# Performance work log

Measured on AMD Instinct MI355X. Metric: run time of the kernel, lower is better.

## Reference

```python
import jax, jax.numpy as jnp
import numpy as np

B, L, DIM, H = 1, 2048, 1536, 12
HD = DIM // H  # 128
SCALE = HD ** -0.5


def quantize_dequant_int8(t):
    # per-tensor symmetric int8 quantize then float dequantize (same math as torch ref)
    s = jnp.max(jnp.abs(t)) / 127.0
    q = jnp.clip(jnp.round(t / s), -128.0, 127.0)
    return q * s


def setup_inputs() -> dict:
    key = jax.random.key(0)
    ks = jax.random.split(key, 6)
    std = DIM ** -0.5
    return {
        "x": jax.random.normal(ks[0], (B, L, DIM), jnp.float32),
        "Wq": jax.random.normal(ks[1], (DIM, DIM), jnp.float32) * std,
        "Wk": jax.random.normal(ks[2], (DIM, DIM), jnp.float32) * std,
        "Wv": jax.random.normal(ks[3], (DIM, DIM), jnp.float32) * std,
        "Wo": jax.random.normal(ks[4], (DIM, DIM), jnp.float32) * std,
        "bo": jax.random.normal(ks[5], (DIM,), jnp.float32) * 0.01,
    }


def reference(x, Wq, Wk, Wv, Wo, bo):
    b, l, c = x.shape
    # QKV projections (torch Linear: x @ W^T), reshape to [B,H,L,HD]
    q = (x @ Wq.T).reshape(b, l, H, HD).transpose(0, 2, 1, 3)
    k = (x @ Wk.T).reshape(b, l, H, HD).transpose(0, 2, 1, 3)
    v = (x @ Wv.T).reshape(b, l, H, HD).transpose(0, 2, 1, 3)
    # sage-style quantize/dequant around both matmuls
    qd = quantize_dequant_int8(q)
    kd = quantize_dequant_int8(k)
    scores = jnp.einsum('bhqd,bhkd->bhqk', qd, kd) * SCALE
    probs = jax.nn.softmax(scores, axis=-1)
    pd = quantize_dequant_int8(probs)
    vd = quantize_dequant_int8(v)
    out = jnp.einsum('bhqk,bhkd->bhqd', pd, vd)  # [B,H,L,HD]
    out = out.transpose(0, 2, 1, 3).reshape(b, l, c)
    return out @ Wo.T + bo
```

## Files before the change

### kernel.cpp

```cpp
#include <hip/hip_runtime.h>
#include <stdint.h>

#define SEQ 2048
#define DIM 1536
#define NH  12
#define HD  128
#define SCALEF 0.08838834764831845f
#define LDP 40

typedef __attribute__((ext_vector_type(8))) short short8;
typedef __attribute__((ext_vector_type(4))) float floatx4;

#define MFMA16(a, b, c) __builtin_amdgcn_mfma_f32_16x16x32_bf16((a), (b), (c), 0, 0, 0)

__device__ __forceinline__ void async_cp16(const void* g, void* l) {
  __builtin_amdgcn_global_load_lds(
      (__attribute__((address_space(1))) unsigned int*)(g),
      (__attribute__((address_space(3))) unsigned int*)(l), 16, 0, 0);
}

__device__ __forceinline__ unsigned short f2bf(float f) {
  unsigned int u = __float_as_uint(f);
  u = (u + 0x7fff + ((u >> 16) & 1)) >> 16;
  return (unsigned short)u;
}

__device__ __forceinline__ void split8v(const float* x, short8& h, short8& l) {
#pragma unroll
  for (int e = 0; e < 8; e++) {
    unsigned int u = __float_as_uint(x[e]);
    h[e] = (short)(u >> 16);
    float r = x[e] - __uint_as_float(u & 0xFFFF0000u);
    l[e] = (short)f2bf(r);
  }
}
__device__ __forceinline__ void split8(const float* g, short8& h, short8& l) {
  float4 f0 = *(const float4*)g, f1 = *(const float4*)(g + 4);
  float x[8] = {f0.x, f0.y, f0.z, f0.w, f1.x, f1.y, f1.z, f1.w};
  split8v(x, h, l);
}

__global__ __launch_bounds__(256) void k_fill(float* __restrict__ out, int n,
                                              float val) {
  int i = blockIdx.x * 256 + threadIdx.x;
  if (i < n) out[i] = val;
}

__global__ __launch_bounds__(256) void k_split_x(
    const float* __restrict__ X, unsigned short* __restrict__ Xh,
    unsigned short* __restrict__ Xl) {
  size_t i = ((size_t)blockIdx.x * 256 + threadIdx.x) * 8;
  short8 h, l;
  split8(X + i, h, l);
  *(short8*)(Xh + i) = h;
  *(short8*)(Xl + i) = l;
}

__global__ __launch_bounds__(256) void k_split_o(
    const float* __restrict__ A0, const float* __restrict__ A1,
    unsigned short* __restrict__ Oh, unsigned short* __restrict__ Ol) {
  size_t i = ((size_t)blockIdx.x * 256 + threadIdx.x) * 8;
  float4 x0 = *(const float4*)(A0 + i), x1 = *(const float4*)(A0 + i + 4);
  float4 y0 = *(const float4*)(A1 + i), y1 = *(const float4*)(A1 + i + 4);
  float xs[8] = {x0.x + y0.x, x0.y + y0.y, x0.z + y0.z, x0.w + y0.w,
                 x1.x + y1.x, x1.y + y1.y, x1.z + y1.z, x1.w + y1.w};
  short8 h, l;
  split8v(xs, h, l);
  *(short8*)(Oh + i) = h;
  *(short8*)(Ol + i) = l;
}

__global__ __launch_bounds__(256) void k_gemm_qkv(
    const unsigned short* __restrict__ Xh, const unsigned short* __restrict__ Xl,
    const float* __restrict__ Wq, const float* __restrict__ Wk,
    const float* __restrict__ Wv, float* __restrict__ qf,
    float* __restrict__ kf, float* __restrict__ vf,
    unsigned int* __restrict__ scal) {
  __shared__ __align__(16) unsigned short Ahs[2][128 * 32], Als[2][128 * 32];
  __shared__ __align__(16) unsigned short Bh[2][128 * LDP], Bl[2][128 * LDP];
  int tid = threadIdx.x, z = blockIdx.z;
  const float* W = (z == 0) ? Wq : (z == 1) ? Wk : Wv;
  float* C = (z == 0) ? qf : (z == 1) ? kf : vf;
  int n0 = blockIdx.x * 128, m0 = blockIdx.y * 128;
  int lane = tid & 63, w = tid >> 6;
  int wr = w >> 1, wc = w & 1, lm = lane & 15, q = lane >> 4;

  floatx4 acc[4][4];
#pragma unroll
  for (int i = 0; i < 4; i++)
#pragma unroll
    for (int j = 0; j < 4; j++) acc[i][j] = (floatx4){0.f, 0.f, 0.f, 0.f};

  int rowA = tid >> 2, c8 = tid & 3;
  const float* pB0 = W + (size_t)(n0 + rowA) * DIM + c8 * 8;
  const float* pB1 = pB0 + (size_t)64 * DIM;
  int sidx0 = tid, sidx1 = 256 + tid;
  int smr0 = sidx0 >> 2, sq0 = (sidx0 & 3) ^ ((smr0 >> 1) & 3);
  int smr1 = sidx1 >> 2, sq1 = (sidx1 & 3) ^ ((smr1 >> 1) & 3);
  size_t gofA0 = (size_t)(m0 + smr0) * DIM + sq0 * 8;
  size_t gofA1 = (size_t)(m0 + smr1) * DIM + sq1 * 8;
  int phA = (q ^ ((lm >> 1) & 3)) * 8;
  int mrbase = wr * 64 + lm;

  {
    async_cp16(Xh + gofA0, &Ahs[0][0] + sidx0 * 8);
    async_cp16(Xl + gofA0, &Als[0][0] + sidx0 * 8);
    async_cp16(Xh + gofA1, &Ahs[0][0] + sidx1 * 8);
    async_cp16(Xl + gofA1, &Als[0][0] + sidx1 * 8);
    short8 h, l;
    split8(pB0, h, l);
    *(short8*)(&Bh[0][0] + rowA * LDP + c8 * 8) = h;
    *(short8*)(&Bl[0][0] + rowA * LDP + c8 * 8) = l;
    split8(pB1, h, l);
    *(short8*)(&Bh[0][0] + (64 + rowA) * LDP + c8 * 8) = h;
    *(short8*)(&Bl[0][0] + (64 + rowA) * LDP + c8 * 8) = l;
  }
  __syncthreads();

  for (int it = 0; it < 47; ++it) {
    int cur = it & 1, nxt = cur ^ 1;
    int kn = it * 32 + 32;
    float4 b00 = *(const float4*)(pB0 + kn);
    float4 b01 = *(const float4*)(pB0 + kn + 4);
    float4 b10 = *(const float4*)(pB1 + kn);
    float4 b11 = *(const float4*)(pB1 + kn + 4);
    async_cp16(Xh + gofA0 + kn, &Ahs[nxt][0] + sidx0 * 8);
    async_cp16(Xl + gofA0 + kn, &Als[nxt][0] + sidx0 * 8);
    async_cp16(Xh + gofA1 + kn, &Ahs[nxt][0] + sidx1 * 8);
    async_cp16(Xl + gofA1 + kn, &Als[nxt][0] + sidx1 * 8);
    short8 ah[4], al[4], bh[4], bl[4];
#pragma unroll
    for (int i = 0; i < 4; i++) {
      int off = (mrbase + i * 16) * 32 + phA;
      ah[i] = *(const short8*)(&Ahs[cur][0] + off);
      al[i] = *(const short8*)(&Als[cur][0] + off);
    }
#pragma unroll
    for (int j = 0; j < 4; j++) {
      int r = wc * 64 + j * 16 + lm;
      bh[j] = *(const short8*)(&Bh[cur][0] + r * LDP + q * 8);
      bl[j] = *(const short8*)(&Bl[cur][0] + r * LDP + q * 8);
    }
#pragma unroll
    for (int i = 0; i < 4; i++)
#pragma unroll
      for (int j = 0; j < 4; j++) {
        acc[i][j] = MFMA16(ah[i], bh[j], acc[i][j]);
        acc[i][j] = MFMA16(ah[i], bl[j], acc[i][j]);
        acc[i][j] = MFMA16(al[i], bh[j], acc[i][j]);
      }
    {
      short8 h, l;
      {
        float xs[8] = {b00.x, b00.y, b00.z, b00.w, b01.x, b01.y, b01.z, b01.w};
        split8v(xs, h, l);
        *(short8*)(&Bh[nxt][0] + rowA * LDP + c8 * 8) = h;
        *(short8*)(&Bl[nxt][0] + rowA * LDP + c8 * 8) = l;
      }
      {
        float xs[8] = {b10.x, b10.y, b10.z, b10.w, b11.x, b11.y, b11.z, b11.w};
        split8v(xs, h, l);
        *(short8*)(&Bh[nxt][0] + (64 + rowA) * LDP + c8 * 8) = h;
        *(short8*)(&Bl[nxt][0] + (64 + rowA) * LDP + c8 * 8) = l;
      }
    }
    __syncthreads();
  }
  {
    short8 ah[4], al[4], bh[4], bl[4];
#pragma unroll
    for (int i = 0; i < 4; i++) {
      int off = (mrbase + i * 16) * 32 + phA;
      ah[i] = *(const short8*)(&Ahs[1][0] + off);
      al[i] = *(const short8*)(&Als[1][0] + off);
    }
#pragma unroll
    for (int j = 0; j < 4; j++) {
      int r = wc * 64 + j * 16 + lm;
      bh[j] = *(const short8*)(&Bh[1][0] + r * LDP + q * 8);
      bl[j] = *(const short8*)(&Bl[1][0] + r * LDP + q * 8);
    }
#pragma unroll
    for (int i = 0; i < 4; i++)
#pragma unroll
      for (int j = 0; j < 4; j++) {
        acc[i][j] = MFMA16(ah[i], bh[j], acc[i][j]);
        acc[i][j] = MFMA16(ah[i], bl[j], acc[i][j]);
        acc[i][j] = MFMA16(al[i], bh[j], acc[i][j]);
      }
  }
  float am = 0.f;
#pragma unroll
  for (int i = 0; i < 4; i++) {
    int row = m0 + wr * 64 + i * 16 + q * 4;
#pragma unroll
    for (int j = 0; j < 4; j++) {
      int col = n0 + wc * 64 + j * 16 + lm;
#pragma unroll
      for (int r = 0; r < 4; r++) {
        float v = acc[i][j][r];
        C[(size_t)(row + r) * DIM + col] = v;
        am = fmaxf(am, fabsf(v));
      }
    }
  }
#pragma unroll
  for (int mk = 32; mk >= 1; mk >>= 1) am = fmaxf(am, __shfl_xor(am, mk, 64));
  if (lane == 0) atomicMax(&scal[z], __float_as_uint(am));
}

__global__ __launch_bounds__(256) void k_quant_vT(
    const float* __restrict__ vf, const unsigned int* __restrict__ scal,
    unsigned short* __restrict__ nvT) {
  __shared__ float T[64 * 65];
  int h = blockIdx.z, d0 = blockIdx.y * 64, k0 = blockIdx.x * 64;
  float s = __uint_as_float(scal[2]) / 127.f;
  int t = threadIdx.x;
#pragma unroll
  for (int i = 0; i < 16; i++) {
    int idx = i * 256 + t;
    int r = idx >> 6, c = idx & 63;
    float v = vf[(size_t)(k0 + r) * DIM + h * HD + d0 + c];
    T[r * 65 + c] = fminf(fmaxf(rintf(v / s), -128.f), 127.f);
  }
  __syncthreads();
#pragma unroll
  for (int i = 0; i < 16; i++) {
    int idx = i * 256 + t;
    int d = idx >> 6, r = idx & 63;
    nvT[(size_t)(h * HD + d0 + d) * SEQ + k0 + r] = f2bf(T[r * 65 + d]);
  }
}

__global__ __launch_bounds__(256) void k_quant_qk(
    const float* __restrict__ qf, const float* __restrict__ kf,
    const unsigned int* __restrict__ scal,
    unsigned short* __restrict__ nq, unsigned short* __restrict__ nk) {
  int z = blockIdx.y;
  const float* src = z ? kf : qf;
  unsigned short* dst = z ? nk : nq;
  float s = __uint_as_float(scal[z]) / 127.f;
  size_t i = ((size_t)blockIdx.x * 256 + threadIdx.x) * 4;
  float4 v = *(const float4*)(src + i);
  ushort4 o;
  o.x = f2bf(fminf(fmaxf(rintf(v.x / s), -128.f), 127.f));
  o.y = f2bf(fminf(fmaxf(rintf(v.y / s), -128.f), 127.f));
  o.z = f2bf(fminf(fmaxf(rintf(v.z / s), -128.f), 127.f));
  o.w = f2bf(fminf(fmaxf(rintf(v.w / s), -128.f), 127.f));
  *(ushort4*)(dst + i) = o;
}

__global__ __launch_bounds__(256) void k_stats(
    const unsigned short* __restrict__ nq, const unsigned short* __restrict__ nk,
    const unsigned int* __restrict__ scal, float* __restrict__ pstats) {
  __shared__ unsigned short Ks[32 * 128];
  int h = blockIdx.y, tid = threadIdx.x, lane = tid & 63, w = tid >> 6;
  int lm = lane & 15, q = lane >> 4;
  int qb = blockIdx.x & 15, chunk = blockIdx.x >> 4;
  int mb = qb * 128 + w * 32;
  int kbase = chunk * 256;
  float f = (__uint_as_float(scal[0]) / 127.f) *
            (__uint_as_float(scal[1]) / 127.f) * SCALEF;

  short8 aq[2][4];
#pragma unroll
  for (int mi = 0; mi < 2; mi++) {
    const unsigned short* qb_p =
        nq + (size_t)(mb + mi * 16 + lm) * DIM + h * HD + q * 8;
#pragma unroll
    for (int cc = 0; cc < 4; cc++) aq[mi][cc] = *(const short8*)(qb_p + cc * 32);
  }

  float m[2][4], zz[2][4];
#pragma unroll
  for (int mi = 0; mi < 2; mi++)
#pragma unroll
    for (int r = 0; r < 4; r++) { m[mi][r] = -3.0e38f; zz[mi][r] = 0.f; }

  for (int kt = kbase; kt < kbase + 256; kt += 32) {
    __syncthreads();
#pragma unroll
    for (int i = 0; i < 2; i++) {
      int ch = i * 256 + tid;
      int krow = ch >> 4;
      int gcol = (ch & 15) ^ (krow & 7);
      async_cp16(nk + (size_t)(kt + krow) * DIM + h * HD + gcol * 8,
                 Ks + ch * 8);
    }
    __syncthreads();
    short8 bk[2][4];
#pragma unroll
    for (int st = 0; st < 2; st++)
#pragma unroll
      for (int cc = 0; cc < 4; cc++) {
        int phys = (cc * 4 + q) ^ (lm & 7);
        bk[st][cc] = *(const short8*)(Ks + (st * 16 + lm) * 128 + phys * 8);
      }
#pragma unroll
    for (int mi = 0; mi < 2; mi++) {
      floatx4 a0 = (floatx4){0.f, 0.f, 0.f, 0.f};
      floatx4 a1 = (floatx4){0.f, 0.f, 0.f, 0.f};
#pragma unroll
      for (int cc = 0; cc < 4; cc++) {
        a0 = MFMA16(aq[mi][cc], bk[0][cc], a0);
        a1 = MFMA16(aq[mi][cc], bk[1][cc], a1);
      }
#pragma unroll
      for (int r = 0; r < 4; r++) {
        float s0 = a0[r] * f, s1 = a1[r] * f;
        float nm = fmaxf(m[mi][r], fmaxf(s0, s1));
        zz[mi][r] = zz[mi][r] * expf(m[mi][r] - nm) + expf(s0 - nm) +
                    expf(s1 - nm);
        m[mi][r] = nm;
      }
    }
  }
#pragma unroll
  for (int mk = 1; mk < 16; mk <<= 1)
#pragma unroll
    for (int mi = 0; mi < 2; mi++)
#pragma unroll
      for (int r = 0; r < 4; r++) {
        float om = __shfl_xor(m[mi][r], mk, 64);
        float oz = __shfl_xor(zz[mi][r], mk, 64);
        float nm = fmaxf(m[mi][r], om);
        zz[mi][r] = zz[mi][r] * expf(m[mi][r] - nm) + oz * expf(om - nm);
        m[mi][r] = nm;
      }
  if (lm == 0) {
#pragma unroll
    for (int mi = 0; mi < 2; mi++)
#pragma unroll
      for (int r = 0; r < 4; r++) {
        int row = mb + mi * 16 + q * 4 + r;
        float* p = pstats + (((size_t)h * SEQ + row) * 8 + chunk) * 2;
        p[0] = m[mi][r];
        p[1] = zz[mi][r];
      }
  }
}

__global__ __launch_bounds__(256) void k_merge(
    const float* __restrict__ pstats, float* __restrict__ stats,
    unsigned int* __restrict__ minZ) {
  int idx = blockIdx.x * 256 + threadIdx.x;
  const float* p = pstats + (size_t)idx * 16;
  float M = -3.0e38f;
#pragma unroll
  for (int c = 0; c < 8; c++) M = fmaxf(M, p[c * 2]);
  float Z = 0.f;
#pragma unroll
  for (int c = 0; c < 8; c++) Z += p[c * 2 + 1] * expf(p[c * 2] - M);
  stats[(size_t)idx * 2] = M;
  stats[(size_t)idx * 2 + 1] = Z;
  atomicMin(minZ, __float_as_uint(Z));
}

__global__ __launch_bounds__(256) void k_attn(
    const unsigned short* __restrict__ nq, const unsigned short* __restrict__ nk,
    const unsigned short* __restrict__ nvT,
    const unsigned int* __restrict__ scal, const unsigned int* __restrict__ minZ,
    const float* __restrict__ stats, float* __restrict__ attn0,
    float* __restrict__ attn1) {
  __shared__ unsigned short Ks[32 * 128];
  __shared__ unsigned short Vs[128 * 32];
  __shared__ unsigned short Pl[4][2][16 * 40];
  int h = blockIdx.y, tid = threadIdx.x, lane = tid & 63, w = tid >> 6;
  int lm = lane & 15, q = lane >> 4;
  int qb = blockIdx.x & 15, chunk = blockIdx.x >> 4;
  int mb = qb * 128 + w * 32;
  float* attn = chunk ? attn1 : attn0;
  float sv = __uint_as_float(scal[2]) / 127.f;
  float f = (__uint_as_float(scal[0]) / 127.f) *
            (__uint_as_float(scal[1]) / 127.f) * SCALEF;
  float sp = (1.f / __uint_as_float(*minZ)) / 127.f;
  float inv_sp = 1.f / sp;

  short8 aq[2][4];
#pragma unroll
  for (int mi = 0; mi < 2; mi++) {
    const unsigned short* qb_p =
        nq + (size_t)(mb + mi * 16 + lm) * DIM + h * HD + q * 8;
#pragma unroll
    for (int cc = 0; cc < 4; cc++) aq[mi][cc] = *(const short8*)(qb_p + cc * 32);
  }
  float M[2][4], invZ[2][4];
#pragma unroll
  for (int mi = 0; mi < 2; mi++)
#pragma unroll
    for (int r = 0; r < 4; r++) {
      int row = mb + mi * 16 + q * 4 + r;
      M[mi][r] = stats[((size_t)h * SEQ + row) * 2];
      invZ[mi][r] = 1.f / stats[((size_t)h * SEQ + row) * 2 + 1];
    }
  floatx4 accO[2][8];
#pragma unroll
  for (int mi = 0; mi < 2; mi++)
#pragma unroll
    for (int j = 0; j < 8; j++) accO[mi][j] = (floatx4){0.f, 0.f, 0.f, 0.f};

  int kbase = chunk * 1024;
  for (int kt = kbase; kt < kbase + 1024; kt += 32) {
    __syncthreads();
#pragma unroll
    for (int i = 0; i < 2; i++) {
      int ch = i * 256 + tid;
      int krow = ch >> 4;
      int gcol = (ch & 15) ^ (krow & 7);
      async_cp16(nk + (size_t)(kt + krow) * DIM + h * HD + gcol * 8,
                 Ks + ch * 8);
      int d = ch >> 2;
      int vcol = (ch & 3) ^ ((d >> 1) & 3);
      async_cp16(nvT + (size_t)(h * HD + d) * SEQ + kt + vcol * 8,
                 Vs + ch * 8);
    }
    __syncthreads();
    short8 bk[2][4];
#pragma unroll
    for (int st = 0; st < 2; st++)
#pragma unroll
      for (int cc = 0; cc < 4; cc++) {
        int phys = (cc * 4 + q) ^ (lm & 7);
        bk[st][cc] = *(const short8*)(Ks + (st * 16 + lm) * 128 + phys * 8);
      }
#pragma unroll
    for (int mi = 0; mi < 2; mi++)
#pragma unroll
      for (int st = 0; st < 2; st++) {
        floatx4 acc = (floatx4){0.f, 0.f, 0.f, 0.f};
#pragma unroll
        for (int cc = 0; cc < 4; cc++) acc = MFMA16(aq[mi][cc], bk[st][cc], acc);
#pragma unroll
        for (int r = 0; r < 4; r++) {
          float t = expf(acc[r] * f - M[mi][r]);
          float n = rintf(t * invZ[mi][r] * inv_sp);
          n = fminf(n, 127.f);
          Pl[w][mi][(q * 4 + r) * 40 + st * 16 + lm] = f2bf(n);
        }
      }
    __syncthreads();
    short8 ap[2];
#pragma unroll
    for (int mi = 0; mi < 2; mi++)
      ap[mi] = *(const short8*)(&Pl[w][mi][lm * 40 + q * 8]);
#pragma unroll
    for (int j = 0; j < 8; j++) {
      int d = j * 16 + lm;
      int vphys = q ^ ((d >> 1) & 3);
      short8 bv = *(const short8*)(Vs + d * 32 + vphys * 8);
#pragma unroll
      for (int mi = 0; mi < 2; mi++) accO[mi][j] = MFMA16(ap[mi], bv, accO[mi][j]);
    }
  }
  float osc = sp * sv;
#pragma unroll
  for (int mi = 0; mi < 2; mi++)
#pragma unroll
    for (int j = 0; j < 8; j++)
#pragma unroll
      for (int r = 0; r < 4; r++)
        attn[(size_t)(mb + mi * 16 + q * 4 + r) * DIM + h * HD + j * 16 + lm] =
            accO[mi][j][r] * osc;
}

__global__ __launch_bounds__(256) void k_gemm_out(
    const unsigned short* __restrict__ Oh, const unsigned short* __restrict__ Ol,
    const float* __restrict__ Wo, const float* __restrict__ bo,
    float* __restrict__ out) {
  __shared__ __align__(16) unsigned short Ahs[2][128 * 32], Als[2][128 * 32];
  __shared__ __align__(16) unsigned short Bh[2][128 * LDP], Bl[2][128 * LDP];
  int tid = threadIdx.x;
  int n0 = blockIdx.x * 128, m0 = blockIdx.y * 128;
  int lane = tid & 63, w = tid >> 6;
  int wr = w >> 1, wc = w & 1, lm = lane & 15, q = lane >> 4;

  floatx4 acc[4][4];
#pragma unroll
  for (int i = 0; i < 4; i++)
#pragma unroll
    for (int j = 0; j < 4; j++) acc[i][j] = (floatx4){0.f, 0.f, 0.f, 0.f};

  int rowA = tid >> 2, c8 = tid & 3;
  const float* pB0 = Wo + (size_t)(n0 + rowA) * DIM + c8 * 8;
  const float* pB1 = pB0 + (size_t)64 * DIM;
  int sidx0 = tid, sidx1 = 256 + tid;
  int smr0 = sidx0 >> 2, sq0 = (sidx0 & 3) ^ ((smr0 >> 1) & 3);
  int smr1 = sidx1 >> 2, sq1 = (sidx1 & 3) ^ ((smr1 >> 1) & 3);
  size_t gofA0 = (size_t)(m0 + smr0) * DIM + sq0 * 8;
  size_t gofA1 = (size_t)(m0 + smr1) * DIM + sq1 * 8;
  int phA = (q ^ ((lm >> 1) & 3)) * 8;
  int mrbase = wr * 64 + lm;

  {
    async_cp16(Oh + gofA0, &Ahs[0][0] + sidx0 * 8);
    async_cp16(Ol + gofA0, &Als[0][0] + sidx0 * 8);
    async_cp16(Oh + gofA1, &Ahs[0][0] + sidx1 * 8);
    async_cp16(Ol + gofA1, &Als[0][0] + sidx1 * 8);
    short8 h, l;
    split8(pB0, h, l);
    *(short8*)(&Bh[0][0] + rowA * LDP + c8 * 8) = h;
    *(short8*)(&Bl[0][0] + rowA * LDP + c8 * 8) = l;
    split8(pB1, h, l);
    *(short8*)(&Bh[0][0] + (64 + rowA) * LDP + c8 * 8) = h;
    *(short8*)(&Bl[0][0] + (64 + rowA) * LDP + c8 * 8) = l;
  }
  __syncthreads();

  for (int it = 0; it < 47; ++it) {
    int cur = it & 1, nxt = cur ^ 1;
    int kn = it * 32 + 32;
    float4 b00 = *(const float4*)(pB0 + kn);
    float4 b01 = *(const float4*)(pB0 + kn + 4);
    float4 b10 = *(const float4*)(pB1 + kn);
    float4 b11 = *(const float4*)(pB1 + kn + 4);
    async_cp16(Oh + gofA0 + kn, &Ahs[nxt][0] + sidx0 * 8);
    async_cp16(Ol + gofA0 + kn, &Als[nxt][0] + sidx0 * 8);
    async_cp16(Oh + gofA1 + kn, &Ahs[nxt][0] + sidx1 * 8);
    async_cp16(Ol + gofA1 + kn, &Als[nxt][0] + sidx1 * 8);
    short8 ah[4], al[4], bh[4], bl[4];
#pragma unroll
    for (int i = 0; i < 4; i++) {
      int off = (mrbase + i * 16) * 32 + phA;
      ah[i] = *(const short8*)(&Ahs[cur][0] + off);
      al[i] = *(const short8*)(&Als[cur][0] + off);
    }
#pragma unroll
    for (int j = 0; j < 4; j++) {
      int r = wc * 64 + j * 16 + lm;
      bh[j] = *(const short8*)(&Bh[cur][0] + r * LDP + q * 8);
      bl[j] = *(const short8*)(&Bl[cur][0] + r * LDP + q * 8);
    }
#pragma unroll
    for (int i = 0; i < 4; i++)
#pragma unroll
      for (int j = 0; j < 4; j++) {
        acc[i][j] = MFMA16(ah[i], bh[j], acc[i][j]);
        acc[i][j] = MFMA16(ah[i], bl[j], acc[i][j]);
        acc[i][j] = MFMA16(al[i], bh[j], acc[i][j]);
      }
    {
      short8 h, l;
      {
        float xs[8] = {b00.x, b00.y, b00.z, b00.w, b01.x, b01.y, b01.z, b01.w};
        split8v(xs, h, l);
        *(short8*)(&Bh[nxt][0] + rowA * LDP + c8 * 8) = h;
        *(short8*)(&Bl[nxt][0] + rowA * LDP + c8 * 8) = l;
      }
      {
        float xs[8] = {b10.x, b10.y, b10.z, b10.w, b11.x, b11.y, b11.z, b11.w};
        split8v(xs, h, l);
        *(short8*)(&Bh[nxt][0] + (64 + rowA) * LDP + c8 * 8) = h;
        *(short8*)(&Bl[nxt][0] + (64 + rowA) * LDP + c8 * 8) = l;
      }
    }
    __syncthreads();
  }
  {
    short8 ah[4], al[4], bh[4], bl[4];
#pragma unroll
    for (int i = 0; i < 4; i++) {
      int off = (mrbase + i * 16) * 32 + phA;
      ah[i] = *(const short8*)(&Ahs[1][0] + off);
      al[i] = *(const short8*)(&Als[1][0] + off);
    }
#pragma unroll
    for (int j = 0; j < 4; j++) {
      int r = wc * 64 + j * 16 + lm;
      bh[j] = *(const short8*)(&Bh[1][0] + r * LDP + q * 8);
      bl[j] = *(const short8*)(&Bl[1][0] + r * LDP + q * 8);
    }
#pragma unroll
    for (int i = 0; i < 4; i++)
#pragma unroll
      for (int j = 0; j < 4; j++) {
        acc[i][j] = MFMA16(ah[i], bh[j], acc[i][j]);
        acc[i][j] = MFMA16(ah[i], bl[j], acc[i][j]);
        acc[i][j] = MFMA16(al[i], bh[j], acc[i][j]);
      }
  }
#pragma unroll
  for (int j = 0; j < 4; j++) {
    int col = n0 + wc * 64 + j * 16 + lm;
    float bias = bo[col];
#pragma unroll
    for (int i = 0; i < 4; i++) {
      int row = m0 + wr * 64 + i * 16 + q * 4;
#pragma unroll
      for (int r = 0; r < 4; r++)
        out[(size_t)(row + r) * DIM + col] = acc[i][j][r] + bias;
    }
  }
}

extern "C" void kernel_launch(void* const* d_in, const int* in_sizes, int n_in,
                              void* d_out, int out_size, void* d_ws, size_t ws_size,
                              hipStream_t stream) {
  float* out = (float*)d_out;
  bool sizes_ok = (n_in >= 6) && in_sizes && in_sizes[0] == SEQ * DIM &&
                  in_sizes[1] == DIM * DIM && in_sizes[2] == DIM * DIM &&
                  in_sizes[3] == DIM * DIM && in_sizes[4] == DIM * DIM &&
                  in_sizes[5] == DIM && out_size == SEQ * DIM;
  if (!sizes_ok) {
    k_fill<<<(out_size + 255) / 256, 256, 0, stream>>>(out, out_size, 1.0f);
    return;
  }
  if (ws_size < 50528272) {
    k_fill<<<(out_size + 255) / 256, 256, 0, stream>>>(out, out_size, 2.0f);
    return;
  }

  const float* x  = (const float*)d_in[0];
  const float* Wq = (const float*)d_in[1];
  const float* Wk = (const float*)d_in[2];
  const float* Wv = (const float*)d_in[3];
  const float* Wo = (const float*)d_in[4];
  const float* bo = (const float*)d_in[5];
  char* ws = (char*)d_ws;

  float* qf = (float*)(ws);
  float* kf = (float*)(ws + 12582912);
  float* vf = (float*)(ws + 25165824);
  unsigned short* nq  = (unsigned short*)(ws + 25165824);
  float* pstats = (float*)(ws + 31457280);
  unsigned short* nvT = (unsigned short*)(ws + 37748736);
  unsigned short* nk  = (unsigned short*)(ws + 44040192);
  unsigned short* Xh = nvT;
  unsigned short* Xl = nk;
  unsigned short* Oh = nvT;
  unsigned short* Ol = nk;
  float* attn0 = qf;
  float* attn1 = kf;
  float* stats = (float*)(ws + 50331648);
  unsigned int* scal = (unsigned int*)(ws + 50528256);

  hipMemsetAsync(scal, 0, 12, stream);
  hipMemsetAsync(scal + 3, 0x7f, 4, stream);

  k_split_x<<<dim3(SEQ * DIM / 2048), 256, 0, stream>>>(x, Xh, Xl);
  k_gemm_qkv<<<dim3(DIM / 128, SEQ / 128, 3), 256, 0, stream>>>(
      Xh, Xl, Wq, Wk, Wv, qf, kf, vf, scal);
  k_quant_vT<<<dim3(SEQ / 64, HD / 64, NH), 256, 0, stream>>>(vf, scal, nvT);
  k_quant_qk<<<dim3((SEQ * DIM) / 1024, 2), 256, 0, stream>>>(qf, kf, scal, nq, nk);
  k_stats<<<dim3(8 * 16, NH), 256, 0, stream>>>(nq, nk, scal, pstats);
  k_merge<<<dim3(NH * SEQ / 256), 256, 0, stream>>>(pstats, stats, scal + 3);
  k_attn<<<dim3(2 * 16, NH), 256, 0, stream>>>(nq, nk, nvT, scal, scal + 3,
                                               stats, attn0, attn1);
  k_split_o<<<dim3(SEQ * DIM / 2048), 256, 0, stream>>>(attn0, attn1, Oh, Ol);
  k_gemm_out<<<dim3(DIM / 128, SEQ / 128), 256, 0, stream>>>(Oh, Ol, Wo, bo, out);
}
```

Baseline: 525.5 us.

## Pre-tile split bf16 activations and remap GEMM block order for locality

The split kernels now write the hi/lo bf16 activations in a tile-contiguous layout, with each 128x32 tile stored contiguously and already XOR-swizzled. The GEMM A-tile async loads therefore read one contiguous 8KB chunk per K step instead of strided rows. Both GEMMs also remap their linear block index so that blocks resident together share M row tiles, which should improve L2 reuse of A and W. The cost is extra index arithmetic and a layout that is no longer row-major for these buffers.

New measurement: 529.6 us. No clear change (+0.8%).

```diff
diff --git a/kernel.cpp b/kernel.cpp
--- a/kernel.cpp
+++ b/kernel.cpp
@@ -49,25 +49,40 @@
 __global__ __launch_bounds__(256) void k_split_x(
     const float* __restrict__ X, unsigned short* __restrict__ Xh,
     unsigned short* __restrict__ Xl) {
-  size_t i = ((size_t)blockIdx.x * 256 + threadIdx.x) * 8;
-  short8 h, l;
-  split8(X + i, h, l);
-  *(short8*)(Xh + i) = h;
-  *(short8*)(Xl + i) = l;
+  int ks = blockIdx.x, mb = blockIdx.y, tid = threadIdx.x;
+  size_t tb = ((size_t)mb * 48 + ks) * 4096;
+#pragma unroll
+  for (int i = 0; i < 2; i++) {
+    int sidx = i * 256 + tid;
+    int row = sidx >> 2, p = sidx & 3;
+    int c = p ^ ((row >> 1) & 3);
+    short8 h, l;
+    split8(X + (size_t)(mb * 128 + row) * DIM + ks * 32 + c * 8, h, l);
+    *(short8*)(Xh + tb + sidx * 8) = h;
+    *(short8*)(Xl + tb + sidx * 8) = l;
+  }
 }
 
 __global__ __launch_bounds__(256) void k_split_o(
     const float* __restrict__ A0, const float* __restrict__ A1,
     unsigned short* __restrict__ Oh, unsigned short* __restrict__ Ol) {
-  size_t i = ((size_t)blockIdx.x * 256 + threadIdx.x) * 8;
-  float4 x0 = *(const float4*)(A0 + i), x1 = *(const float4*)(A0 + i + 4);
-  float4 y0 = *(const float4*)(A1 + i), y1 = *(const float4*)(A1 + i + 4);
-  float xs[8] = {x0.x + y0.x, x0.y + y0.y, x0.z + y0.z, x0.w + y0.w,
-                 x1.x + y1.x, x1.y + y1.y, x1.z + y1.z, x1.w + y1.w};
-  short8 h, l;
-  split8v(xs, h, l);
-  *(short8*)(Oh + i) = h;
-  *(short8*)(Ol + i) = l;
+  int ks = blockIdx.x, mb = blockIdx.y, tid = threadIdx.x;
+  size_t tb = ((size_t)mb * 48 + ks) * 4096;
+#pragma unroll
+  for (int i = 0; i < 2; i++) {
+    int sidx = i * 256 + tid;
+    int row = sidx >> 2, p = sidx & 3;
+    int c = p ^ ((row >> 1) & 3);
+    size_t off = (size_t)(mb * 128 + row) * DIM + ks * 32 + c * 8;
+    float4 x0 = *(const float4*)(A0 + off), x1 = *(const float4*)(A0 + off + 4);
+    float4 y0 = *(const float4*)(A1 + off), y1 = *(const float4*)(A1 + off + 4);
+    float xs[8] = {x0.x + y0.x, x0.y + y0.y, x0.z + y0.z, x0.w + y0.w,
+                   x1.x + y1.x, x1.y + y1.y, x1.z + y1.z, x1.w + y1.w};
+    short8 h, l;
+    split8v(xs, h, l);
+    *(short8*)(Oh + tb + sidx * 8) = h;
+    *(short8*)(Ol + tb + sidx * 8) = l;
+  }
 }
 
 __global__ __launch_bounds__(256) void k_gemm_qkv(
@@ -78,10 +93,14 @@
     unsigned int* __restrict__ scal) {
   __shared__ __align__(16) unsigned short Ahs[2][128 * 32], Als[2][128 * 32];
   __shared__ __align__(16) unsigned short Bh[2][128 * LDP], Bl[2][128 * LDP];
-  int tid = threadIdx.x, z = blockIdx.z;
+  int tid = threadIdx.x;
+  int L = blockIdx.x + 12 * blockIdx.y + 192 * blockIdx.z;
+  int L2 = (L & 7) * 72 + (L >> 3);
+  int by2 = L2 & 15, rest = L2 >> 4;
+  int bx2 = rest % 12, z = rest / 12;
   const float* W = (z == 0) ? Wq : (z == 1) ? Wk : Wv;
   float* C = (z == 0) ? qf : (z == 1) ? kf : vf;
-  int n0 = blockIdx.x * 128, m0 = blockIdx.y * 128;
+  int n0 = bx2 * 128, m0 = by2 * 128;
   int lane = tid & 63, w = tid >> 6;
   int wr = w >> 1, wc = w & 1, lm = lane & 15, q = lane >> 4;
 
@@ -94,19 +113,16 @@
   int rowA = tid >> 2, c8 = tid & 3;
   const float* pB0 = W + (size_t)(n0 + rowA) * DIM + c8 * 8;
   const float* pB1 = pB0 + (size_t)64 * DIM;
+  size_t tb = (size_t)by2 * 48 * 4096;
   int sidx0 = tid, sidx1 = 256 + tid;
-  int smr0 = sidx0 >> 2, sq0 = (sidx0 & 3) ^ ((smr0 >> 1) & 3);
-  int smr1 = sidx1 >> 2, sq1 = (sidx1 & 3) ^ ((smr1 >> 1) & 3);
-  size_t gofA0 = (size_t)(m0 + smr0) * DIM + sq0 * 8;
-  size_t gofA1 = (size_t)(m0 + smr1) * DIM + sq1 * 8;
   int phA = (q ^ ((lm >> 1) & 3)) * 8;
   int mrbase = wr * 64 + lm;
 
   {
-    async_cp16(Xh + gofA0, &Ahs[0][0] + sidx0 * 8);
-    async_cp16(Xl + gofA0, &Als[0][0] + sidx0 * 8);
-    async_cp16(Xh + gofA1, &Ahs[0][0] + sidx1 * 8);
-    async_cp16(Xl + gofA1, &Als[0][0] + sidx1 * 8);
+    async_cp16(Xh + tb + sidx0 * 8, &Ahs[0][0] + sidx0 * 8);
+    async_cp16(Xl + tb + sidx0 * 8, &Als[0][0] + sidx0 * 8);
+    async_cp16(Xh + tb + sidx1 * 8, &Ahs[0][0] + sidx1 * 8);
+    async_cp16(Xl + tb + sidx1 * 8, &Als[0][0] + sidx1 * 8);
     short8 h, l;
     split8(pB0, h, l);
     *(short8*)(&Bh[0][0] + rowA * LDP + c8 * 8) = h;
@@ -120,14 +136,15 @@
   for (int it = 0; it < 47; ++it) {
     int cur = it & 1, nxt = cur ^ 1;
     int kn = it * 32 + 32;
+    size_t tn = tb + (size_t)(it + 1) * 4096;
     float4 b00 = *(const float4*)(pB0 + kn);
     float4 b01 = *(const float4*)(pB0 + kn + 4);
     float4 b10 = *(const float4*)(pB1 + kn);
     float4 b11 = *(const float4*)(pB1 + kn + 4);
-    async_cp16(Xh + gofA0 + kn, &Ahs[nxt][0] + sidx0 * 8);
-    async_cp16(Xl + gofA0 + kn, &Als[nxt][0] + sidx0 * 8);
-    async_cp16(Xh + gofA1 + kn, &Ahs[nxt][0] + sidx1 * 8);
-    async_cp16(Xl + gofA1 + kn, &Als[nxt][0] + sidx1 * 8);
+    async_cp16(Xh + tn + sidx0 * 8, &Ahs[nxt][0] + sidx0 * 8);
+    async_cp16(Xl + tn + sidx0 * 8, &Als[nxt][0] + sidx0 * 8);
+    async_cp16(Xh + tn + sidx1 * 8, &Ahs[nxt][0] + sidx1 * 8);
+    async_cp16(Xl + tn + sidx1 * 8, &Als[nxt][0] + sidx1 * 8);
     short8 ah[4], al[4], bh[4], bl[4];
 #pragma unroll
     for (int i = 0; i < 4; i++) {
@@ -470,7 +487,10 @@
   __shared__ __align__(16) unsigned short Ahs[2][128 * 32], Als[2][128 * 32];
   __shared__ __align__(16) unsigned short Bh[2][128 * LDP], Bl[2][128 * LDP];
   int tid = threadIdx.x;
-  int n0 = blockIdx.x * 128, m0 = blockIdx.y * 128;
+  int L = blockIdx.x + 12 * blockIdx.y;
+  int L2 = (L & 7) * 24 + (L >> 3);
+  int by2 = L2 & 15, bx2 = L2 >> 4;
+  int n0 = bx2 * 128, m0 = by2 * 128;
   int lane = tid & 63, w = tid >> 6;
   int wr = w >> 1, wc = w & 1, lm = lane & 15, q = lane >> 4;
 
@@ -483,19 +503,16 @@
   int rowA = tid >> 2, c8 = tid & 3;
   const float* pB0 = Wo + (size_t)(n0 + rowA) * DIM + c8 * 8;
   const float* pB1 = pB0 + (size_t)64 * DIM;
+  size_t tb = (size_t)by2 * 48 * 4096;
   int sidx0 = tid, sidx1 = 256 + tid;
-  int smr0 = sidx0 >> 2, sq0 = (sidx0 & 3) ^ ((smr0 >> 1) & 3);
-  int smr1 = sidx1 >> 2, sq1 = (sidx1 & 3) ^ ((smr1 >> 1) & 3);
-  size_t gofA0 = (size_t)(m0 + smr0) * DIM + sq0 * 8;
-  size_t gofA1 = (size_t)(m0 + smr1) * DIM + sq1 * 8;
   int phA = (q ^ ((lm >> 1) & 3)) * 8;
   int mrbase = wr * 64 + lm;
 
   {
-    async_cp16(Oh + gofA0, &Ahs[0][0] + sidx0 * 8);
-    async_cp16(Ol + gofA0, &Als[0][0] + sidx0 * 8);
-    async_cp16(Oh + gofA1, &Ahs[0][0] + sidx1 * 8);
-    async_cp16(Ol + gofA1, &Als[0][0] + sidx1 * 8);
+    async_cp16(Oh + tb + sidx0 * 8, &Ahs[0][0] + sidx0 * 8);
+    async_cp16(Ol + tb + sidx0 * 8, &Als[0][0] + sidx0 * 8);
+    async_cp16(Oh + tb + sidx1 * 8, &Ahs[0][0] + sidx1 * 8);
+    async_cp16(Ol + tb + sidx1 * 8, &Als[0][0] + sidx1 * 8);
     short8 h, l;
     split8(pB0, h, l);
     *(short8*)(&Bh[0][0] + rowA * LDP + c8 * 8) = h;
@@ -509,14 +526,15 @@
   for (int it = 0; it < 47; ++it) {
     int cur = it & 1, nxt = cur ^ 1;
     int kn = it * 32 + 32;
+    size_t tn = tb + (size_t)(it + 1) * 4096;
     float4 b00 = *(const float4*)(pB0 + kn);
     float4 b01 = *(const float4*)(pB0 + kn + 4);
     float4 b10 = *(const float4*)(pB1 + kn);
     float4 b11 = *(const float4*)(pB1 + kn + 4);
-    async_cp16(Oh + gofA0 + kn, &Ahs[nxt][0] + sidx0 * 8);
-    async_cp16(Ol + gofA0 + kn, &Als[nxt][0] + sidx0 * 8);
-    async_cp16(Oh + gofA1 + kn, &Ahs[nxt][0] + sidx1 * 8);
-    async_cp16(Ol + gofA1 + kn, &Als[nxt][0] + sidx1 * 8);
+    async_cp16(Oh + tn + sidx0 * 8, &Ahs[nxt][0] + sidx0 * 8);
+    async_cp16(Ol + tn + sidx0 * 8, &Als[nxt][0] + sidx0 * 8);
+    async_cp16(Oh + tn + sidx1 * 8, &Ahs[nxt][0] + sidx1 * 8);
+    async_cp16(Ol + tn + sidx1 * 8, &Als[nxt][0] + sidx1 * 8);
     short8 ah[4], al[4], bh[4], bl[4];
 #pragma unroll
     for (int i = 0; i < 4; i++) {
@@ -636,7 +654,7 @@
   hipMemsetAsync(scal, 0, 12, stream);
   hipMemsetAsync(scal + 3, 0x7f, 4, stream);
 
-  k_split_x<<<dim3(SEQ * DIM / 2048), 256, 0, stream>>>(x, Xh, Xl);
+  k_split_x<<<dim3(48, 16), 256, 0, stream>>>(x, Xh, Xl);
   k_gemm_qkv<<<dim3(DIM / 128, SEQ / 128, 3), 256, 0, stream>>>(
       Xh, Xl, Wq, Wk, Wv, qf, kf, vf, scal);
   k_quant_vT<<<dim3(SEQ / 64, HD / 64, NH), 256, 0, stream>>>(vf, scal, nvT);
@@ -645,6 +663,6 @@
   k_merge<<<dim3(NH * SEQ / 256), 256, 0, stream>>>(pstats, stats, scal + 3);
   k_attn<<<dim3(2 * 16, NH), 256, 0, stream>>>(nq, nk, nvT, scal, scal + 3,
                                                stats, attn0, attn1);
-  k_split_o<<<dim3(SEQ * DIM / 2048), 256, 0, stream>>>(attn0, attn1, Oh, Ol);
+  k_split_o<<<dim3(48, 16), 256, 0, stream>>>(attn0, attn1, Oh, Ol);
   k_gemm_out<<<dim3(DIM / 128, SEQ / 128), 256, 0, stream>>>(Oh, Ol, Wo, bo, out);
 }
```
